# Optimization experiments

Hardware: AMD Instinct MI355X
Metric: run time of the kernel (lower is better)

The kernel has to match this reference:

```python
import jax, jax.numpy as jnp
import numpy as np

Z_DIM = 2  # state dimension is hard-coded (fc1: Linear(2, H), fc3: Linear(H, 2))


def _mlp(z, W1, b1, W2, b2, W3, b3):
    # torch.nn.Linear: y = x @ W.T + b
    h = jax.nn.elu(z @ W1.T + b1)
    h = jax.nn.elu(h @ W2.T + b2)
    return h @ W3.T + b3


def setup_inputs() -> dict:
    key = jax.random.key(0)
    ks = jax.random.split(key, 8)
    B, H = 1_000_000, 64
    s_in = 1.0 / np.sqrt(Z_DIM)
    s_h = 1.0 / np.sqrt(H)
    u = lambda k, shp, s: jax.random.uniform(k, shp, jnp.float32, -s, s)
    return {
        "t": jax.random.normal(ks[0], (1,), jnp.float32),
        "z_and_logp": jax.random.normal(ks[1], (B, Z_DIM + 1), jnp.float32),
        "W1": u(ks[2], (H, Z_DIM), s_in),
        "b1": u(ks[3], (H,), s_in),
        "W2": u(ks[4], (H, H), s_h),
        "b2": u(ks[5], (H,), s_h),
        "W3": u(ks[6], (Z_DIM, H), s_h),
        "b3": u(ks[7], (Z_DIM,), s_h),
    }


def reference(t, z_and_logp, W1, b1, W2, b2, W3, b3):
    # t is an unused time argument (ODE solver interface).
    z = z_and_logp[:, :Z_DIM]  # [B, 2]; logp column is not used in forward
    f = lambda x: _mlp(x, W1, b1, W2, b2, W3, b3)

    # Exact Jacobian trace via forward-mode JVPs with unit tangents (Z_DIM=2,
    # so this small fixed loop mirrors the per-dim autograd loop in torch).
    dz_dt = None
    trace = jnp.zeros(z.shape[0], dtype=z.dtype)
    for i in range(Z_DIM):
        e = jnp.zeros_like(z).at[:, i].set(1.0)
        out, jz = jax.jvp(f, (z,), (e,))
        if dz_dt is None:
            dz_dt = out
        trace = trace + jz[:, i]

    dlogp_dt = -trace[:, None]  # [B, 1]
    return jnp.concatenate([dz_dt, dlogp_dt], axis=1)  # [B, 3]
```

## Files before the change

kernel.cpp:

```cpp
#include <hip/hip_runtime.h>
#include <hip/hip_fp16.h>


typedef _Float16 f16x8 __attribute__((ext_vector_type(8)));
typedef _Float16 f16x2 __attribute__((ext_vector_type(2)));
typedef float    f32x4 __attribute__((ext_vector_type(4)));

static __device__ __forceinline__ f16x8 exp2_h8(f16x8 t) {
    f16x8 e;
#pragma unroll
    for (int p = 0; p < 4; ++p) {
        f16x2 t2 = {t[2*p], t[2*p+1]};
        __half2 r = h2exp2(__builtin_bit_cast(__half2, t2));
        f16x2 e2 = __builtin_bit_cast(f16x2, r);
        e[2*p] = e2[0]; e[2*p+1] = e2[1];
    }
    return e;
}

static __device__ __forceinline__ f16x2 exp2_h2(f16x2 t) {
    __half2 r = h2exp2(__builtin_bit_cast(__half2, t));
    return __builtin_bit_cast(f16x2, r);
}

static __device__ __forceinline__ f16x2 cvtpk(float a, float b) {
    return __builtin_bit_cast(f16x2, __builtin_amdgcn_cvt_pkrtz(a, b));
}

static __device__ __forceinline__ f16x2 shfl_xor_h2(f16x2 v, int m) {
    int u = __shfl_xor(__builtin_bit_cast(int, v), m);
    return __builtin_bit_cast(f16x2, u);
}

__global__ __launch_bounds__(256) __attribute__((amdgpu_waves_per_eu(2, 2)))
void odefunc_mfma(const float* __restrict__ zin,
                  const float* __restrict__ W1, const float* __restrict__ b1,
                  const float* __restrict__ W2, const float* __restrict__ b2,
                  const float* __restrict__ W3, const float* __restrict__ b3,
                  float* __restrict__ out, int B, int ntiles)
{
    const float L2E  = 1.442695040888963f;
    const float RL2E = 0.6931471805599453f;

    __shared__ _Float16 sH[192];
    __shared__ f32x4    sC[48];

    const int lane = threadIdx.x & 63;
    const int quad = lane >> 4;
    const int col  = lane & 15;

    if (threadIdx.x < 64) {
        int i = threadIdx.x;
        sH[i]       = (_Float16)(W1[2*i]     * L2E);
        sH[64 + i]  = (_Float16)(W1[2*i + 1] * L2E);
        sH[128 + i] = (_Float16)(b1[i]       * L2E);
        float* s = (float*)sC;
        s[i]       = b2[i] * L2E;
        s[64 + i]  = W3[i]      * RL2E;
        s[128 + i] = W3[64 + i] * RL2E;
    }

    const int wid    = blockIdx.x * (blockDim.x >> 6) + (threadIdx.x >> 6);
    const int nwaves = gridDim.x * (blockDim.x >> 6);

    f16x8 aW2[4][2], aG[4][2];
#pragma unroll
    for (int mt = 0; mt < 4; ++mt) {
        const int k = mt * 16 + col;
        const float ck = W3[k], dk = W3[64 + k];
#pragma unroll
        for (int jt = 0; jt < 2; ++jt) {
            const float* p = W2 + k * 64 + jt * 32 + quad * 8;
#pragma unroll
            for (int jj = 0; jj < 8; ++jj) {
                int j = jt * 32 + quad * 8 + jj;
                float w2 = p[jj];
                aW2[mt][jt][jj] = (_Float16)w2;
                aG[mt][jt][jj]  = (_Float16)(w2 * fmaf(ck, W1[2*j], dk * W1[2*j+1]));
            }
        }
    }

    const float b30 = b3[0], b31 = b3[1];
    const f32x4 zero4 = {0.f, 0.f, 0.f, 0.f};
    const _Float16 hl2e = (_Float16)L2E;
    const _Float16 h0   = (_Float16)0.0f;
    const f16x8 zero8 = {h0,h0,h0,h0,h0,h0,h0,h0};
    const f16x8 l2e8  = {hl2e,hl2e,hl2e,hl2e,hl2e,hl2e,hl2e,hl2e};
    const f16x8 ml2e8 = {-hl2e,-hl2e,-hl2e,-hl2e,-hl2e,-hl2e,-hl2e,-hl2e};
    const f16x2 zero2 = {h0, h0};
    const f16x2 l2e2  = {hl2e, hl2e};
    const f16x2 ml2e2 = {-hl2e, -hl2e};

    __syncthreads();

    f16x8 cw0[2], cw1[2], cbb[2];
#pragma unroll
    for (int jt = 0; jt < 2; ++jt) {
        int j0 = jt * 32 + quad * 8;
        cw0[jt] = *(const f16x8*)(sH + j0);
        cw1[jt] = *(const f16x8*)(sH + j0 + 64);
        cbb[jt] = *(const f16x8*)(sH + j0 + 128);
    }
    f32x4 cb2[4];
    f16x2 cw30h[4][2], cw31h[4][2];
#pragma unroll
    for (int mt = 0; mt < 4; ++mt) {
        int k4 = mt * 4 + quad;
        cb2[mt] = sC[k4];
        f32x4 w30 = sC[k4 + 16];
        f32x4 w31 = sC[k4 + 32];
        cw30h[mt][0] = cvtpk(w30[0], w30[1]);
        cw30h[mt][1] = cvtpk(w30[2], w30[3]);
        cw31h[mt][0] = cvtpk(w31[0], w31[1]);
        cw31h[mt][1] = cvtpk(w31[2], w31[3]);
    }

    int tp = wid;
    float z0A = 0.f, z1A = 0.f, z0B = 0.f, z1B = 0.f;
    if (2 * tp < ntiles) {
        int rA = (2 * tp) * 16 + col;
        z0A = zin[3 * rA];  z1A = zin[3 * rA + 1];
        if (2 * tp + 1 < ntiles) {
            int rB = (2 * tp + 1) * 16 + col;
            z0B = zin[3 * rB];  z1B = zin[3 * rB + 1];
        }
    }

    for (; 2 * tp < ntiles; tp += nwaves) {
        const int tA = 2 * tp, tB = 2 * tp + 1;
        const bool vB = tB < ntiles;

        int tpn = tp + nwaves;
        int rAn = ((2 * tpn     < ntiles) ? 2 * tpn     : 0) * 16 + col;
        int rBn = ((2 * tpn + 1 < ntiles) ? 2 * tpn + 1 : 0) * 16 + col;
        float z0An = zin[3 * rAn], z1An = zin[3 * rAn + 1];
        float z0Bn = zin[3 * rBn], z1Bn = zin[3 * rBn + 1];

        const _Float16 z0Ah = (_Float16)z0A, z1Ah = (_Float16)z1A;
        const _Float16 z0Bh = (_Float16)z0B, z1Bh = (_Float16)z1B;
        const f16x8 z0A8 = {z0Ah,z0Ah,z0Ah,z0Ah,z0Ah,z0Ah,z0Ah,z0Ah};
        const f16x8 z1A8 = {z1Ah,z1Ah,z1Ah,z1Ah,z1Ah,z1Ah,z1Ah,z1Ah};
        const f16x8 z0B8 = {z0Bh,z0Bh,z0Bh,z0Bh,z0Bh,z0Bh,z0Bh,z0Bh};
        const f16x8 z1B8 = {z1Bh,z1Bh,z1Bh,z1Bh,z1Bh,z1Bh,z1Bh,z1Bh};

        f16x8 BhA[2], BeA[2], BhB[2], BeB[2];
#pragma unroll
        for (int jt = 0; jt < 2; ++jt) {
            f16x8 aA = __builtin_elementwise_fma(cw0[jt], z0A8,
                       __builtin_elementwise_fma(cw1[jt], z1A8, cbb[jt]));
            f16x8 eA = exp2_h8(__builtin_elementwise_min(aA, zero8));
            f16x8 hA = __builtin_elementwise_max(aA,
                       __builtin_elementwise_fma(l2e8, eA, ml2e8));
            f16x8 aB = __builtin_elementwise_fma(cw0[jt], z0B8,
                       __builtin_elementwise_fma(cw1[jt], z1B8, cbb[jt]));
            f16x8 eB = exp2_h8(__builtin_elementwise_min(aB, zero8));
            f16x8 hB = __builtin_elementwise_max(aB,
                       __builtin_elementwise_fma(l2e8, eB, ml2e8));
            BhA[jt] = hA; BeA[jt] = eA;
            BhB[jt] = hB; BeB[jt] = eB;
        }

        f32x4 aHA[4], aTA[4], aHB[4], aTB[4];
#pragma unroll
        for (int mt = 0; mt < 4; ++mt) {
            aHA[mt] = __builtin_amdgcn_mfma_f32_16x16x32_f16(aW2[mt][0], BhA[0], cb2[mt], 0, 0, 0);
            aHA[mt] = __builtin_amdgcn_mfma_f32_16x16x32_f16(aW2[mt][1], BhA[1], aHA[mt], 0, 0, 0);
            aHB[mt] = __builtin_amdgcn_mfma_f32_16x16x32_f16(aW2[mt][0], BhB[0], cb2[mt], 0, 0, 0);
            aHB[mt] = __builtin_amdgcn_mfma_f32_16x16x32_f16(aW2[mt][1], BhB[1], aHB[mt], 0, 0, 0);
            aTA[mt] = __builtin_amdgcn_mfma_f32_16x16x32_f16(aG[mt][0], BeA[0], zero4, 0, 0, 0);
            aTA[mt] = __builtin_amdgcn_mfma_f32_16x16x32_f16(aG[mt][1], BeA[1], aTA[mt], 0, 0, 0);
            aTB[mt] = __builtin_amdgcn_mfma_f32_16x16x32_f16(aG[mt][0], BeB[0], zero4, 0, 0, 0);
            aTB[mt] = __builtin_amdgcn_mfma_f32_16x16x32_f16(aG[mt][1], BeB[1], aTB[mt], 0, 0, 0);
        }

        f16x2 o0A2 = zero2, o1A2 = zero2, trA2 = zero2;
        f16x2 o0B2 = zero2, o1B2 = zero2, trB2 = zero2;
#pragma unroll
        for (int mt = 0; mt < 4; ++mt) {
#pragma unroll
            for (int p = 0; p < 2; ++p) {
                f16x2 w30p = cw30h[mt][p], w31p = cw31h[mt][p];
                f16x2 ahA = cvtpk(aHA[mt][2*p], aHA[mt][2*p+1]);
                f16x2 atA = cvtpk(aTA[mt][2*p], aTA[mt][2*p+1]);
                f16x2 eA  = exp2_h2(__builtin_elementwise_min(ahA, zero2));
                f16x2 hhA = __builtin_elementwise_max(ahA,
                            __builtin_elementwise_fma(l2e2, eA, ml2e2));
                o0A2 = __builtin_elementwise_fma(w30p, hhA, o0A2);
                o1A2 = __builtin_elementwise_fma(w31p, hhA, o1A2);
                trA2 = __builtin_elementwise_fma(eA, atA, trA2);
                f16x2 ahB = cvtpk(aHB[mt][2*p], aHB[mt][2*p+1]);
                f16x2 atB = cvtpk(aTB[mt][2*p], aTB[mt][2*p+1]);
                f16x2 eB  = exp2_h2(__builtin_elementwise_min(ahB, zero2));
                f16x2 hhB = __builtin_elementwise_max(ahB,
                            __builtin_elementwise_fma(l2e2, eB, ml2e2));
                o0B2 = __builtin_elementwise_fma(w30p, hhB, o0B2);
                o1B2 = __builtin_elementwise_fma(w31p, hhB, o1B2);
                trB2 = __builtin_elementwise_fma(eB, atB, trB2);
            }
        }

        f16x2 pA  = { (_Float16)(o0A2[0] + o0A2[1]), (_Float16)(o1A2[0] + o1A2[1]) };
        f16x2 pB  = { (_Float16)(o0B2[0] + o0B2[1]), (_Float16)(o1B2[0] + o1B2[1]) };
        f16x2 pT  = { (_Float16)(trA2[0] + trA2[1]), (_Float16)(trB2[0] + trB2[1]) };
        pA += shfl_xor_h2(pA, 16);  pA += shfl_xor_h2(pA, 32);
        pB += shfl_xor_h2(pB, 16);  pB += shfl_xor_h2(pB, 32);
        pT += shfl_xor_h2(pT, 16);  pT += shfl_xor_h2(pT, 32);

        int rowA = tA * 16 + col;
        if (lane < 16 && rowA < B) {
            out[3 * rowA + 0] = (float)pA[0] + b30;
            out[3 * rowA + 1] = (float)pA[1] + b31;
            out[3 * rowA + 2] = -(float)pT[0];
        }
        int rowB = tB * 16 + col;
        if (lane < 16 && vB && rowB < B) {
            out[3 * rowB + 0] = (float)pB[0] + b30;
            out[3 * rowB + 1] = (float)pB[1] + b31;
            out[3 * rowB + 2] = -(float)pT[1];
        }

        z0A = z0An; z1A = z1An;
        z0B = z0Bn; z1B = z1Bn;
    }
}

extern "C" void kernel_launch(void* const* d_in, const int* in_sizes, int n_in,
                              void* d_out, int out_size, void* d_ws, size_t ws_size,
                              hipStream_t stream) {
    const float* zin = (const float*)d_in[1];
    const float* W1  = (const float*)d_in[2];
    const float* b1  = (const float*)d_in[3];
    const float* W2  = (const float*)d_in[4];
    const float* b2  = (const float*)d_in[5];
    const float* W3  = (const float*)d_in[6];
    const float* b3  = (const float*)d_in[7];
    float* out = (float*)d_out;

    int B = in_sizes[1] / 3;
    int ntiles = (B + 15) / 16;
    int grid = 512;
    odefunc_mfma<<<grid, 256, 0, stream>>>(zin, W1, b1, W2, b2, W3, b3,
                                           out, B, ntiles);
}
```

Before: 113.6 us.

## Move b2/W3 constants to LDS reloads to reach three waves per EU

Stops holding the layer-2 bias and packed W3 weights in registers across the loop. Each iteration now reloads them from shared memory, and an opaque offset keeps the compiler from hoisting those loads back out. The freed VGPRs let the occupancy target rise from 2 to 3 waves per EU, and the grid grows from 512 to 768 blocks to match. The cost is extra LDS loads inside the hot loop.

```diff
diff --git a/kernel.cpp b/kernel.cpp
--- a/kernel.cpp
+++ b/kernel.cpp
@@ -32,7 +32,7 @@
     return __builtin_bit_cast(f16x2, u);
 }
 
-__global__ __launch_bounds__(256) __attribute__((amdgpu_waves_per_eu(2, 2)))
+__global__ __launch_bounds__(256) __attribute__((amdgpu_waves_per_eu(3, 3)))
 void odefunc_mfma(const float* __restrict__ zin,
                   const float* __restrict__ W1, const float* __restrict__ b1,
                   const float* __restrict__ W2, const float* __restrict__ b2,
@@ -43,7 +43,9 @@
     const float RL2E = 0.6931471805599453f;
 
     __shared__ _Float16 sH[192];
-    __shared__ f32x4    sC[48];
+    __shared__ f32x4    sB2[16];
+    __shared__ f16x2    sW30h[32];
+    __shared__ f16x2    sW31h[32];
 
     const int lane = threadIdx.x & 63;
     const int quad = lane >> 4;
@@ -54,10 +56,12 @@
         sH[i]       = (_Float16)(W1[2*i]     * L2E);
         sH[64 + i]  = (_Float16)(W1[2*i + 1] * L2E);
         sH[128 + i] = (_Float16)(b1[i]       * L2E);
-        float* s = (float*)sC;
-        s[i]       = b2[i] * L2E;
-        s[64 + i]  = W3[i]      * RL2E;
-        s[128 + i] = W3[64 + i] * RL2E;
+        ((float*)sB2)[i] = b2[i] * L2E;
+        if (i < 32) {
+            int kk = ((i >> 3) * 4 + ((i >> 1) & 3)) * 4 + 2 * (i & 1);
+            sW30h[i] = cvtpk(W3[kk]      * RL2E, W3[kk + 1]      * RL2E);
+            sW31h[i] = cvtpk(W3[64 + kk] * RL2E, W3[64 + kk + 1] * RL2E);
+        }
     }
 
     const int wid    = blockIdx.x * (blockDim.x >> 6) + (threadIdx.x >> 6);
@@ -102,19 +106,6 @@
         cw1[jt] = *(const f16x8*)(sH + j0 + 64);
         cbb[jt] = *(const f16x8*)(sH + j0 + 128);
     }
-    f32x4 cb2[4];
-    f16x2 cw30h[4][2], cw31h[4][2];
-#pragma unroll
-    for (int mt = 0; mt < 4; ++mt) {
-        int k4 = mt * 4 + quad;
-        cb2[mt] = sC[k4];
-        f32x4 w30 = sC[k4 + 16];
-        f32x4 w31 = sC[k4 + 32];
-        cw30h[mt][0] = cvtpk(w30[0], w30[1]);
-        cw30h[mt][1] = cvtpk(w30[2], w30[3]);
-        cw31h[mt][0] = cvtpk(w31[0], w31[1]);
-        cw31h[mt][1] = cvtpk(w31[2], w31[3]);
-    }
 
     int tp = wid;
     float z0A = 0.f, z1A = 0.f, z0B = 0.f, z1B = 0.f;
@@ -127,7 +118,9 @@
         }
     }
 
+    int cofs = 0;
     for (; 2 * tp < ntiles; tp += nwaves) {
+        asm volatile("" : "+v"(cofs));
         const int tA = 2 * tp, tB = 2 * tp + 1;
         const bool vB = tB < ntiles;
 
@@ -164,9 +157,10 @@
         f32x4 aHA[4], aTA[4], aHB[4], aTB[4];
 #pragma unroll
         for (int mt = 0; mt < 4; ++mt) {
-            aHA[mt] = __builtin_amdgcn_mfma_f32_16x16x32_f16(aW2[mt][0], BhA[0], cb2[mt], 0, 0, 0);
+            f32x4 b2v = sB2[cofs + mt * 4 + quad];
+            aHA[mt] = __builtin_amdgcn_mfma_f32_16x16x32_f16(aW2[mt][0], BhA[0], b2v, 0, 0, 0);
             aHA[mt] = __builtin_amdgcn_mfma_f32_16x16x32_f16(aW2[mt][1], BhA[1], aHA[mt], 0, 0, 0);
-            aHB[mt] = __builtin_amdgcn_mfma_f32_16x16x32_f16(aW2[mt][0], BhB[0], cb2[mt], 0, 0, 0);
+            aHB[mt] = __builtin_amdgcn_mfma_f32_16x16x32_f16(aW2[mt][0], BhB[0], b2v, 0, 0, 0);
             aHB[mt] = __builtin_amdgcn_mfma_f32_16x16x32_f16(aW2[mt][1], BhB[1], aHB[mt], 0, 0, 0);
             aTA[mt] = __builtin_amdgcn_mfma_f32_16x16x32_f16(aG[mt][0], BeA[0], zero4, 0, 0, 0);
             aTA[mt] = __builtin_amdgcn_mfma_f32_16x16x32_f16(aG[mt][1], BeA[1], aTA[mt], 0, 0, 0);
@@ -180,7 +174,9 @@
         for (int mt = 0; mt < 4; ++mt) {
 #pragma unroll
             for (int p = 0; p < 2; ++p) {
-                f16x2 w30p = cw30h[mt][p], w31p = cw31h[mt][p];
+                int we = cofs + mt * 8 + quad * 2 + p;
+                f16x2 w30p = sW30h[we];
+                f16x2 w31p = sW31h[we];
                 f16x2 ahA = cvtpk(aHA[mt][2*p], aHA[mt][2*p+1]);
                 f16x2 atA = cvtpk(aTA[mt][2*p], aTA[mt][2*p+1]);
                 f16x2 eA  = exp2_h2(__builtin_elementwise_min(ahA, zero2));
@@ -239,7 +235,7 @@
 
     int B = in_sizes[1] / 3;
     int ntiles = (B + 15) / 16;
-    int grid = 512;
+    int grid = 768;
     odefunc_mfma<<<grid, 256, 0, stream>>>(zin, W1, b1, W2, b2, W3, b3,
                                            out, B, ntiles);
 }
```

Result: slower. 117.6 us (+3.6%).
